# Kernel tuning notes

Measured on AMD Instinct MI355X. Metric: run time of the kernel, lower is better.

## Reference

```python
import jax, jax.numpy as jnp
import numpy as np
import math


def setup_inputs() -> dict:
    key = jax.random.key(0)
    ks = jax.random.split(key, 16)
    B, S, H, K, PREV = 32, 2048, 1024, 4, 2
    sc = 0.02
    return {
        "last_hidden": jax.random.normal(ks[0], (1, B, H), jnp.float32),
        "decoder_inputs": jax.random.normal(ks[1], (B, 1, H), jnp.float32),
        "encoder_outputs": jax.random.normal(ks[2], (B, S, H), jnp.float32),
        "attention_scores": jax.random.normal(ks[3], (PREV, B, 1, S), jnp.float32),
        "attention_mask": jnp.zeros((B, 1, S), jnp.float32),
        "evidence_scores": jax.random.uniform(ks[4], (B,), jnp.float32),
        "evidence_sentence_index": jax.random.randint(ks[5], (B, PREV), 0, S, dtype=jnp.int32),
        "W_ih": jax.random.normal(ks[6], (3 * H, H), jnp.float32) * sc,
        "W_hh": jax.random.normal(ks[7], (3 * H, H), jnp.float32) * sc,
        "b_ih": jax.random.normal(ks[8], (3 * H,), jnp.float32) * sc,
        "b_hh": jax.random.normal(ks[9], (3 * H,), jnp.float32) * sc,
        "Wk": jax.random.normal(ks[10], (H, H), jnp.float32) * sc,
        "bk": jnp.zeros((H,), jnp.float32),
        "Wv": jax.random.normal(ks[11], (H, H), jnp.float32) * sc,
        "bv": jnp.zeros((H,), jnp.float32),
        "topk": K,
    }


def _gru_step(x, h, W_ih, W_hh, b_ih, b_hh):
    # x, h: (B, H). PyTorch GRU cell math.
    gi = x @ W_ih.T + b_ih  # (B, 3H)
    gh = h @ W_hh.T + b_hh  # (B, 3H)
    i_r, i_z, i_n = jnp.split(gi, 3, axis=1)
    h_r, h_z, h_n = jnp.split(gh, 3, axis=1)
    r = jax.nn.sigmoid(i_r + h_r)
    z = jax.nn.sigmoid(i_z + h_z)
    n = jnp.tanh(i_n + r * h_n)
    return (1.0 - z) * n + z * h


def reference(last_hidden, decoder_inputs, encoder_outputs, attention_scores,
              attention_mask, evidence_scores, evidence_sentence_index,
              W_ih, W_hh, b_ih, b_hh, Wk, bk, Wv, bv, topk):
    B, S, H = encoder_outputs.shape
    K = topk
    R = B // K  # real batch (beam groups)

    key_eo = encoder_outputs @ Wk.T + bk    # (B, S, H)
    val_eo = encoder_outputs @ Wv.T + bv    # (B, S, H)

    h_new = _gru_step(decoder_inputs[:, 0], last_hidden[0], W_ih, W_hh, b_ih, b_hh)  # (B, H)
    output = h_new[:, None, :]              # (B, 1, H)

    attn_outputs = jnp.einsum('bih,bsh->bis', output, key_eo) / math.sqrt(H) + attention_mask  # (B,1,S)
    attn_alignment = jax.nn.softmax(attn_outputs, axis=-1)
    context = jnp.einsum('bis,bsh->bih', attn_alignment, val_eo)  # (B, 1, H)

    # top-k per beam, then joint rerank over topk*topk candidates per real example
    vals, idx = jax.lax.top_k(attn_alignment.reshape(R, K, S), K)  # (R, K, K), sorted desc
    scores = vals.reshape(B, K)
    sentences = idx.reshape(B, K)
    log_scores = -jnp.log(scores) + evidence_scores[:, None]       # (B, K)

    flat = log_scores.reshape(R, K * K)
    order = jnp.argsort(flat, axis=-1)[:, :K]                      # (R, K) ascending, stable
    new_evidence_scores = jnp.take_along_axis(flat, order, axis=1).reshape(B)
    s_flat = (order // K + jnp.arange(R)[:, None] * K).reshape(B)  # source beam in [0, B)
    r_flat = (order % K).reshape(B)

    sel_sent = sentences[s_flat, r_flat]                           # (B,)
    result = context[s_flat]                                       # (B, 1, H)
    hidden = h_new[s_flat][None]                                   # (1, B, H)
    new_evidence_sentence_index = jnp.concatenate(
        [evidence_sentence_index[s_flat], sel_sent[:, None].astype(evidence_sentence_index.dtype)], axis=1)
    new_attention_scores = jnp.concatenate(
        [attention_scores[:, s_flat], attn_outputs[s_flat][None]], axis=0)  # (prev+1, B, 1, S)
    new_attention_mask = attention_mask[s_flat]                    # (B, 1, S)

    return (result, hidden, new_evidence_sentence_index,
            new_attention_scores, new_attention_mask, new_evidence_scores)
```

## Files before the change

### kernel.cpp

```cpp
#include <hip/hip_runtime.h>
#include <hip/hip_bf16.h>
#include <cfloat>
#include <climits>
#include <cmath>

#define BB 32
#define SS 2048
#define HH 1024
#define KK 4
#define CH 32

__global__ __launch_bounds__(256) void gates_partial(
    const float* __restrict__ x, const float* __restrict__ h_old,
    const float* __restrict__ W_ih, const float* __restrict__ W_hh,
    float* __restrict__ part) {
  int t = threadIdx.x;
  int jb = blockIdx.x;
  int kc = blockIdx.y;
  int bq = blockIdx.z;
  int k0 = kc * 64;
  bool second = (jb >= 12);
  const float* A = (second ? h_old : x) + (size_t)(bq * 8) * HH;
  const float* W = second ? W_hh : W_ih;
  int j0 = jb * 256;
  int jr = j0 - (second ? 3072 : 0);
  const float* wp = W + (size_t)(jr + t) * HH + k0;
  float acc[8];
#pragma unroll
  for (int bi = 0; bi < 8; bi++) acc[bi] = 0.f;
#pragma unroll
  for (int kk = 0; kk < 64; kk += 4) {
    float4 wv = *(const float4*)(wp + kk);
#pragma unroll
    for (int bi = 0; bi < 8; bi++) {
      float4 a = *(const float4*)(A + (size_t)bi * HH + k0 + kk);
      acc[bi] += a.x * wv.x + a.y * wv.y + a.z * wv.z + a.w * wv.w;
    }
  }
  float* pb = part + ((size_t)kc * 32 + bq * 8) * 6144 + j0 + t;
#pragma unroll
  for (int bi = 0; bi < 8; bi++) pb[(size_t)bi * 6144] = acc[bi];
}

__global__ __launch_bounds__(256) void gru_pw(
    const float* __restrict__ part, const float* __restrict__ b_ih,
    const float* __restrict__ b_hh, const float* __restrict__ h_old,
    float* __restrict__ h_new) {
  int t = threadIdx.x;
  int b = blockIdx.x;
  int h = blockIdx.y * 256 + t;
  float s0 = 0.f, s1 = 0.f, s2 = 0.f, s3 = 0.f, s4 = 0.f, s5 = 0.f;
#pragma unroll
  for (int c = 0; c < 16; c++) {
    const float* p = part + ((size_t)c * 32 + b) * 6144;
    s0 += p[h];
    s1 += p[1024 + h];
    s2 += p[2048 + h];
    s3 += p[3072 + h];
    s4 += p[4096 + h];
    s5 += p[5120 + h];
  }
  float ir = s0 + b_ih[h], iz = s1 + b_ih[1024 + h], in_ = s2 + b_ih[2048 + h];
  float hr = s3 + b_hh[h], hz = s4 + b_hh[1024 + h], hn = s5 + b_hh[2048 + h];
  float r = 1.f / (1.f + expf(-(ir + hr)));
  float z = 1.f / (1.f + expf(-(iz + hz)));
  float n = tanhf(in_ + r * hn);
  h_new[b * HH + h] = (1.f - z) * n + z * h_old[b * HH + h];
}

__global__ __launch_bounds__(256) void q_partial(const float* __restrict__ hnew,
                                                 const float* __restrict__ Wk,
                                                 float* __restrict__ qpart) {
  int t = threadIdx.x;
  int n = blockIdx.x * 256 + t;
  int j0 = blockIdx.y * 32;
  int b0 = blockIdx.z * 8;
  float acc[8];
#pragma unroll
  for (int bi = 0; bi < 8; bi++) acc[bi] = 0.f;
#pragma unroll
  for (int j = 0; j < 32; j += 4) {
    float w0 = Wk[(size_t)(j0 + j + 0) * HH + n];
    float w1 = Wk[(size_t)(j0 + j + 1) * HH + n];
    float w2 = Wk[(size_t)(j0 + j + 2) * HH + n];
    float w3 = Wk[(size_t)(j0 + j + 3) * HH + n];
#pragma unroll
    for (int bi = 0; bi < 8; bi++) {
      float4 hv = *(const float4*)(hnew + (size_t)(b0 + bi) * HH + j0 + j);
      acc[bi] += hv.x * w0 + hv.y * w1 + hv.z * w2 + hv.w * w3;
    }
  }
  float* pb = qpart + ((size_t)blockIdx.y * 32 + b0) * 1024 + n;
#pragma unroll
  for (int bi = 0; bi < 8; bi++) pb[(size_t)bi * 1024] = acc[bi];
}

__global__ __launch_bounds__(256) void q_reduce(const float* __restrict__ qpart,
                                                float* __restrict__ q) {
  int t = threadIdx.x;
  int b = blockIdx.x >> 2;
  int n = (blockIdx.x & 3) * 256 + t;
  float s = 0.f;
#pragma unroll
  for (int jc = 0; jc < 32; jc++) s += qpart[((size_t)jc * 32 + b) * 1024 + n];
  q[b * HH + n] = s;
}

__global__ __launch_bounds__(256) void fused_attn(
    const float* __restrict__ eo, const float* __restrict__ q,
    const float* __restrict__ h_new, const float* __restrict__ bk,
    const float* __restrict__ mask, float* __restrict__ logits,
    float* __restrict__ c0part, float* __restrict__ msum_part) {
  __shared__ float q_lds[HH];
  __shared__ float wred[4];
  __shared__ float cacc[4][1024];
  __shared__ float cms[4][2];
  int b = blockIdx.y, sc = blockIdx.x, t = threadIdx.x;
  int w = t >> 6, lane = t & 63;
  {
    float4 qs = *(const float4*)(q + (size_t)b * HH + 4 * t);
    *(float4*)&q_lds[4 * t] = qs;
    float4 hv = *(const float4*)(h_new + (size_t)b * HH + 4 * t);
    float4 kv = *(const float4*)(bk + 4 * t);
    float p = hv.x * kv.x + hv.y * kv.y + hv.z * kv.z + hv.w * kv.w;
#pragma unroll
    for (int off = 32; off; off >>= 1) p += __shfl_xor(p, off);
    if (lane == 0) wred[w] = p;
  }
  __syncthreads();
  float hb = wred[0] + wred[1] + wred[2] + wred[3];
  float4 qv[4];
#pragma unroll
  for (int i = 0; i < 4; i++) qv[i] = *(const float4*)&q_lds[(i * 64 + lane) * 4];

  float m = -FLT_MAX, sum = 0.f;
  float4 acc[4];
#pragma unroll
  for (int i = 0; i < 4; i++) acc[i] = make_float4(0.f, 0.f, 0.f, 0.f);
  int rbase = sc * 64 + w * 16;
  for (int tile = 0; tile < 8; tile++) {
    int r0 = rbase + tile * 2;
    float4 rv[2][4];
#pragma unroll
    for (int rr = 0; rr < 2; rr++) {
      const float4* e4 = (const float4*)(eo + ((size_t)b * SS + r0 + rr) * HH);
#pragma unroll
      for (int i = 0; i < 4; i++) rv[rr][i] = e4[i * 64 + lane];
    }
    float p0 = 0.f, p1 = 0.f;
#pragma unroll
    for (int i = 0; i < 4; i++) {
      p0 += rv[0][i].x * qv[i].x + rv[0][i].y * qv[i].y +
            rv[0][i].z * qv[i].z + rv[0][i].w * qv[i].w;
      p1 += rv[1][i].x * qv[i].x + rv[1][i].y * qv[i].y +
            rv[1][i].z * qv[i].z + rv[1][i].w * qv[i].w;
    }
#pragma unroll
    for (int off = 32; off; off >>= 1) {
      p0 += __shfl_xor(p0, off);
      p1 += __shfl_xor(p1, off);
    }
    float lv0 = (p0 + hb) * 0.03125f + mask[(size_t)b * SS + r0];
    float lv1 = (p1 + hb) * 0.03125f + mask[(size_t)b * SS + r0 + 1];
    if (lane == 0) {
      logits[(size_t)b * SS + r0] = lv0;
      logits[(size_t)b * SS + r0 + 1] = lv1;
    }
    float m_new = fmaxf(m, fmaxf(lv0, lv1));
    float scale = expf(m - m_new);
    float w0 = expf(lv0 - m_new), w1 = expf(lv1 - m_new);
    sum = sum * scale + w0 + w1;
#pragma unroll
    for (int i = 0; i < 4; i++) {
      acc[i].x = acc[i].x * scale + w0 * rv[0][i].x + w1 * rv[1][i].x;
      acc[i].y = acc[i].y * scale + w0 * rv[0][i].y + w1 * rv[1][i].y;
      acc[i].z = acc[i].z * scale + w0 * rv[0][i].z + w1 * rv[1][i].z;
      acc[i].w = acc[i].w * scale + w0 * rv[0][i].w + w1 * rv[1][i].w;
    }
    m = m_new;
  }
#pragma unroll
  for (int i = 0; i < 4; i++) *(float4*)&cacc[w][i * 256 + lane * 4] = acc[i];
  if (lane == 0) { cms[w][0] = m; cms[w][1] = sum; }
  __syncthreads();
  float m0 = cms[0][0], m1 = cms[1][0], m2 = cms[2][0], m3 = cms[3][0];
  float mb = fmaxf(fmaxf(m0, m1), fmaxf(m2, m3));
  float wt0 = expf(m0 - mb), wt1 = expf(m1 - mb), wt2 = expf(m2 - mb),
        wt3 = expf(m3 - mb);
  float sb = cms[0][1] * wt0 + cms[1][1] * wt1 + cms[2][1] * wt2 + cms[3][1] * wt3;
  float4 a0 = *(float4*)&cacc[0][4 * t];
  float4 a1 = *(float4*)&cacc[1][4 * t];
  float4 a2 = *(float4*)&cacc[2][4 * t];
  float4 a3 = *(float4*)&cacc[3][4 * t];
  float4 r;
  r.x = wt0 * a0.x + wt1 * a1.x + wt2 * a2.x + wt3 * a3.x;
  r.y = wt0 * a0.y + wt1 * a1.y + wt2 * a2.y + wt3 * a3.y;
  r.z = wt0 * a0.z + wt1 * a1.z + wt2 * a2.z + wt3 * a3.z;
  r.w = wt0 * a0.w + wt1 * a1.w + wt2 * a2.w + wt3 * a3.w;
  *(float4*)(c0part + ((size_t)sc * 32 + b) * 1024 + 4 * t) = r;
  if (t == 0) {
    msum_part[((size_t)sc * 32 + b) * 2 + 0] = mb;
    msum_part[((size_t)sc * 32 + b) * 2 + 1] = sb;
  }
}

__device__ __forceinline__ bool vi_better(float av, int ai, float bv, int bi) {
  return av > bv || (av == bv && ai < bi);
}

__global__ __launch_bounds__(256) void attn_finish(
    const float* __restrict__ c0part, const float* __restrict__ msum_part,
    const float* __restrict__ logits, float* __restrict__ c0,
    float* __restrict__ scores, int* __restrict__ sent) {
  int bid = blockIdx.x, t = threadIdx.x;
  int b = (bid < 128) ? (bid >> 2) : (bid - 128);
  float m = -FLT_MAX;
  float ms[CH];
#pragma unroll
  for (int c = 0; c < CH; c++) {
    ms[c] = msum_part[((size_t)c * 32 + b) * 2 + 0];
    m = fmaxf(m, ms[c]);
  }
  float sum = 0.f;
  float wc[CH];
#pragma unroll
  for (int c = 0; c < CH; c++) {
    wc[c] = expf(ms[c] - m);
    sum += msum_part[((size_t)c * 32 + b) * 2 + 1] * wc[c];
  }
  float inv = 1.f / sum;

  if (bid < 128) {
    int h = (bid & 3) * 256 + t;
    float a = 0.f;
#pragma unroll
    for (int c = 0; c < CH; c++)
      a += wc[c] * c0part[((size_t)c * 32 + b) * 1024 + h];
    c0[(size_t)b * HH + h] = a * inv;
    return;
  }

  float tv0 = -FLT_MAX, tv1 = -FLT_MAX, tv2 = -FLT_MAX, tv3 = -FLT_MAX;
  int ti0 = INT_MAX, ti1 = INT_MAX, ti2 = INT_MAX, ti3 = INT_MAX;
#pragma unroll
  for (int it = 0; it < 8; it++) {
    int idx = it * 256 + t;
    float v = logits[(size_t)b * SS + idx];
    if (vi_better(v, idx, tv3, ti3)) {
      tv3 = v; ti3 = idx;
      if (vi_better(tv3, ti3, tv2, ti2)) { float fv = tv2; int fi = ti2; tv2 = tv3; ti2 = ti3; tv3 = fv; ti3 = fi; }
      if (vi_better(tv2, ti2, tv1, ti1)) { float fv = tv1; int fi = ti1; tv1 = tv2; ti1 = ti2; tv2 = fv; ti2 = fi; }
      if (vi_better(tv1, ti1, tv0, ti0)) { float fv = tv0; int fi = ti0; tv0 = tv1; ti0 = ti1; tv1 = fv; ti1 = fi; }
    }
  }
  __shared__ float sv[256][4];
  __shared__ int si[256][4];
  sv[t][0] = tv0; sv[t][1] = tv1; sv[t][2] = tv2; sv[t][3] = tv3;
  si[t][0] = ti0; si[t][1] = ti1; si[t][2] = ti2; si[t][3] = ti3;
  __syncthreads();
  for (int off = 128; off; off >>= 1) {
    if (t < off) {
      float bv0 = sv[t + off][0], bv1 = sv[t + off][1], bv2 = sv[t + off][2], bv3 = sv[t + off][3];
      int bi0 = si[t + off][0], bi1 = si[t + off][1], bi2 = si[t + off][2], bi3 = si[t + off][3];
      float mv0, mv1, mv2, mv3; int mi0, mi1, mi2, mi3;
      if (vi_better(tv0, ti0, bv3, bi3)) { mv0 = tv0; mi0 = ti0; } else { mv0 = bv3; mi0 = bi3; }
      if (vi_better(tv1, ti1, bv2, bi2)) { mv1 = tv1; mi1 = ti1; } else { mv1 = bv2; mi1 = bi2; }
      if (vi_better(tv2, ti2, bv1, bi1)) { mv2 = tv2; mi2 = ti2; } else { mv2 = bv1; mi2 = bi1; }
      if (vi_better(tv3, ti3, bv0, bi0)) { mv3 = tv3; mi3 = ti3; } else { mv3 = bv0; mi3 = bi0; }
      if (!vi_better(mv0, mi0, mv2, mi2)) { float fv = mv0; int fi = mi0; mv0 = mv2; mi0 = mi2; mv2 = fv; mi2 = fi; }
      if (!vi_better(mv1, mi1, mv3, mi3)) { float fv = mv1; int fi = mi1; mv1 = mv3; mi1 = mi3; mv3 = fv; mi3 = fi; }
      if (!vi_better(mv0, mi0, mv1, mi1)) { float fv = mv0; int fi = mi0; mv0 = mv1; mi0 = mi1; mv1 = fv; mi1 = fi; }
      if (!vi_better(mv2, mi2, mv3, mi3)) { float fv = mv2; int fi = mi2; mv2 = mv3; mi2 = mi3; mv3 = fv; mi3 = fi; }
      tv0 = mv0; tv1 = mv1; tv2 = mv2; tv3 = mv3;
      ti0 = mi0; ti1 = mi1; ti2 = mi2; ti3 = mi3;
      sv[t][0] = tv0; sv[t][1] = tv1; sv[t][2] = tv2; sv[t][3] = tv3;
      si[t][0] = ti0; si[t][1] = ti1; si[t][2] = ti2; si[t][3] = ti3;
    }
    __syncthreads();
  }
  if (t == 0) {
    scores[b * KK + 0] = expf(tv0 - m) * inv; sent[b * KK + 0] = ti0;
    scores[b * KK + 1] = expf(tv1 - m) * inv; sent[b * KK + 1] = ti1;
    scores[b * KK + 2] = expf(tv2 - m) * inv; sent[b * KK + 2] = ti2;
    scores[b * KK + 3] = expf(tv3 - m) * inv; sent[b * KK + 3] = ti3;
  }
}

__global__ __launch_bounds__(256) void ctx_sel_gather(
    const float* __restrict__ scores, const int* __restrict__ sent,
    const float* __restrict__ evidence, const int* __restrict__ esi,
    const float* __restrict__ Wv, const float* __restrict__ bvec,
    const float* __restrict__ c0, const float* __restrict__ hnew,
    const float* __restrict__ attn_in, const float* __restrict__ logits,
    const float* __restrict__ mask, float* __restrict__ out0,
    float* __restrict__ out1, float* __restrict__ out2,
    float* __restrict__ out3, float* __restrict__ out4,
    float* __restrict__ out5) {
  __shared__ int s_sh;
  __shared__ float cs[HH];
  int jq = blockIdx.x, b = blockIdx.y, t = threadIdx.x;
  if (t == 0) {
    int r = b >> 2, j = b & 3;
    float ls[16];
    bool used[16];
    for (int k1 = 0; k1 < 4; k1++)
      for (int k2 = 0; k2 < 4; k2++)
        ls[k1 * 4 + k2] = -logf(scores[(r * 4 + k1) * 4 + k2]) + evidence[r * 4 + k1];
    for (int i = 0; i < 16; i++) used[i] = false;
    int best = 0;
    float bvv = FLT_MAX;
    for (int jj = 0; jj <= j; jj++) {
      best = 0;
      bvv = FLT_MAX;
      for (int i = 0; i < 16; i++)
        if (!used[i] && ls[i] < bvv) { bvv = ls[i]; best = i; }
      used[best] = true;
    }
    int k1 = best >> 2, k2 = best & 3;
    int sSel = r * 4 + k1;
    s_sh = sSel;
    if (jq == 0) {
      out5[b] = bvv;
      out2[b * 3 + 0] = (float)esi[sSel * 2 + 0];
      out2[b * 3 + 1] = (float)esi[sSel * 2 + 1];
      out2[b * 3 + 2] = (float)sent[sSel * 4 + k2];
    }
  }
  __syncthreads();
  int s = s_sh;
  *(float4*)&cs[4 * t] = *(const float4*)(c0 + (size_t)s * HH + 4 * t);
  __syncthreads();
  {
    int j = jq * 256 + t;
    const float4* w4 = (const float4*)(Wv + (size_t)j * HH);
    float acc = bvec[j];
#pragma unroll 8
    for (int k4 = 0; k4 < 256; k4++) {
      float4 wv = w4[k4];
      float4 cc = *(const float4*)&cs[4 * k4];
      acc += wv.x * cc.x + wv.y * cc.y + wv.z * cc.z + wv.w * cc.w;
    }
    out0[(size_t)b * HH + j] = acc;
  }
  out1[(size_t)b * HH + jq * 256 + t] = hnew[(size_t)s * HH + jq * 256 + t];
#pragma unroll
  for (int p = 0; p < 2; p++) {
    *(float2*)(out3 + ((size_t)p * BB + b) * SS + jq * 512 + 2 * t) =
        *(const float2*)(attn_in + ((size_t)p * BB + s) * SS + jq * 512 + 2 * t);
  }
  *(float2*)(out3 + ((size_t)2 * BB + b) * SS + jq * 512 + 2 * t) =
      *(const float2*)(logits + (size_t)s * SS + jq * 512 + 2 * t);
  *(float2*)(out4 + (size_t)b * SS + jq * 512 + 2 * t) =
      *(const float2*)(mask + (size_t)s * SS + jq * 512 + 2 * t);
}

extern "C" void kernel_launch(void* const* d_in, const int* in_sizes, int n_in,
                              void* d_out, int out_size, void* d_ws, size_t ws_size,
                              hipStream_t stream) {
  const float* h_old = (const float*)d_in[0];
  const float* x     = (const float*)d_in[1];
  const float* eo    = (const float*)d_in[2];
  const float* attn_in = (const float*)d_in[3];
  const float* mask  = (const float*)d_in[4];
  const float* evidence = (const float*)d_in[5];
  const int*   esi   = (const int*)d_in[6];
  const float* W_ih  = (const float*)d_in[7];
  const float* W_hh  = (const float*)d_in[8];
  const float* b_ih  = (const float*)d_in[9];
  const float* b_hh  = (const float*)d_in[10];
  const float* Wk    = (const float*)d_in[11];
  const float* bk    = (const float*)d_in[12];
  const float* Wv    = (const float*)d_in[13];
  const float* bv    = (const float*)d_in[14];

  float* w = (float*)d_ws;
  float* h_new  = w + 0;
  float* q      = w + 32768;
  float* logits = w + 65536;
  float* scores = w + 131072;
  int*   sent   = (int*)(w + 131200);
  float* c0     = w + 131328;
  float* msum_part = w + 164096;
  float* c0part = w + 166144;
  float* gpart  = w + 1214720;
  float* qpart  = w + 4360448;

  float* out0 = (float*)d_out;
  float* out1 = out0 + 32768;
  float* out2 = out1 + 32768;
  float* out3 = out2 + 96;
  float* out4 = out3 + 196608;
  float* out5 = out4 + 65536;

  gates_partial<<<dim3(24, 16, 4), 256, 0, stream>>>(x, h_old, W_ih, W_hh, gpart);
  gru_pw<<<dim3(32, 4), 256, 0, stream>>>(gpart, b_ih, b_hh, h_old, h_new);
  q_partial<<<dim3(4, 32, 4), 256, 0, stream>>>(h_new, Wk, qpart);
  q_reduce<<<128, 256, 0, stream>>>(qpart, q);
  fused_attn<<<dim3(CH, BB), 256, 0, stream>>>(eo, q, h_new, bk, mask, logits,
                                               c0part, msum_part);
  attn_finish<<<160, 256, 0, stream>>>(c0part, msum_part, logits, c0, scores, sent);
  ctx_sel_gather<<<dim3(4, BB), 256, 0, stream>>>(
      scores, sent, evidence, esi, Wv, bv, c0, h_new, attn_in, logits, mask,
      out0, out1, out2, out3, out4, out5);
}
```

Before: 127.5 us.

## Fuse attention finish into selection/context kernel with wave-level top-k

```diff
diff --git a/kernel.cpp b/kernel.cpp
--- a/kernel.cpp
+++ b/kernel.cpp
@@ -208,44 +208,45 @@
   return av > bv || (av == bv && ai < bi);
 }
 
-__global__ __launch_bounds__(256) void attn_finish(
+__global__ __launch_bounds__(256) void tail_sel_ctx(
     const float* __restrict__ c0part, const float* __restrict__ msum_part,
-    const float* __restrict__ logits, float* __restrict__ c0,
-    float* __restrict__ scores, int* __restrict__ sent) {
-  int bid = blockIdx.x, t = threadIdx.x;
-  int b = (bid < 128) ? (bid >> 2) : (bid - 128);
+    const float* __restrict__ logits, const float* __restrict__ evidence,
+    const int* __restrict__ esi, const float* __restrict__ Wv,
+    const float* __restrict__ bvec, const float* __restrict__ hnew,
+    const float* __restrict__ attn_in, const float* __restrict__ mask,
+    float* __restrict__ out0, float* __restrict__ out1,
+    float* __restrict__ out2, float* __restrict__ out3,
+    float* __restrict__ out4, float* __restrict__ out5) {
+  __shared__ float tvs[4][4];
+  __shared__ int tis[4][4];
+  __shared__ float mrow[4], srow[4];
+  __shared__ int s_sh;
+  __shared__ float wc_lds[32];
+  __shared__ float cs[HH];
+  int jq = blockIdx.x, b = blockIdx.y, t = threadIdx.x;
+  int w = t >> 6, lane = t & 63;
+  int r = b >> 2;
+  int row = r * 4 + w;
+
   float m = -FLT_MAX;
-  float ms[CH];
+  float msv[CH];
 #pragma unroll
   for (int c = 0; c < CH; c++) {
-    ms[c] = msum_part[((size_t)c * 32 + b) * 2 + 0];
-    m = fmaxf(m, ms[c]);
+    msv[c] = msum_part[((size_t)c * 32 + row) * 2 + 0];
+    m = fmaxf(m, msv[c]);
   }
   float sum = 0.f;
-  float wc[CH];
-#pragma unroll
-  for (int c = 0; c < CH; c++) {
-    wc[c] = expf(ms[c] - m);
-    sum += msum_part[((size_t)c * 32 + b) * 2 + 1] * wc[c];
-  }
-  float inv = 1.f / sum;
-
-  if (bid < 128) {
-    int h = (bid & 3) * 256 + t;
-    float a = 0.f;
-#pragma unroll
-    for (int c = 0; c < CH; c++)
-      a += wc[c] * c0part[((size_t)c * 32 + b) * 1024 + h];
-    c0[(size_t)b * HH + h] = a * inv;
-    return;
-  }
-
+#pragma unroll
+  for (int c = 0; c < CH; c++)
+    sum += msum_part[((size_t)c * 32 + row) * 2 + 1] * expf(msv[c] - m);
+
+  const float* lrow = logits + (size_t)row * SS;
   float tv0 = -FLT_MAX, tv1 = -FLT_MAX, tv2 = -FLT_MAX, tv3 = -FLT_MAX;
   int ti0 = INT_MAX, ti1 = INT_MAX, ti2 = INT_MAX, ti3 = INT_MAX;
 #pragma unroll
-  for (int it = 0; it < 8; it++) {
-    int idx = it * 256 + t;
-    float v = logits[(size_t)b * SS + idx];
+  for (int it = 0; it < 32; it++) {
+    int idx = it * 64 + lane;
+    float v = lrow[idx];
     if (vi_better(v, idx, tv3, ti3)) {
       tv3 = v; ti3 = idx;
       if (vi_better(tv3, ti3, tv2, ti2)) { float fv = tv2; int fi = ti2; tv2 = tv3; ti2 = ti3; tv3 = fv; ti3 = fi; }
@@ -253,59 +254,42 @@
       if (vi_better(tv1, ti1, tv0, ti0)) { float fv = tv0; int fi = ti0; tv0 = tv1; ti0 = ti1; tv1 = fv; ti1 = fi; }
     }
   }
-  __shared__ float sv[256][4];
-  __shared__ int si[256][4];
-  sv[t][0] = tv0; sv[t][1] = tv1; sv[t][2] = tv2; sv[t][3] = tv3;
-  si[t][0] = ti0; si[t][1] = ti1; si[t][2] = ti2; si[t][3] = ti3;
-  __syncthreads();
-  for (int off = 128; off; off >>= 1) {
-    if (t < off) {
-      float bv0 = sv[t + off][0], bv1 = sv[t + off][1], bv2 = sv[t + off][2], bv3 = sv[t + off][3];
-      int bi0 = si[t + off][0], bi1 = si[t + off][1], bi2 = si[t + off][2], bi3 = si[t + off][3];
-      float mv0, mv1, mv2, mv3; int mi0, mi1, mi2, mi3;
-      if (vi_better(tv0, ti0, bv3, bi3)) { mv0 = tv0; mi0 = ti0; } else { mv0 = bv3; mi0 = bi3; }
-      if (vi_better(tv1, ti1, bv2, bi2)) { mv1 = tv1; mi1 = ti1; } else { mv1 = bv2; mi1 = bi2; }
-      if (vi_better(tv2, ti2, bv1, bi1)) { mv2 = tv2; mi2 = ti2; } else { mv2 = bv1; mi2 = bi1; }
-      if (vi_better(tv3, ti3, bv0, bi0)) { mv3 = tv3; mi3 = ti3; } else { mv3 = bv0; mi3 = bi0; }
-      if (!vi_better(mv0, mi0, mv2, mi2)) { float fv = mv0; int fi = mi0; mv0 = mv2; mi0 = mi2; mv2 = fv; mi2 = fi; }
-      if (!vi_better(mv1, mi1, mv3, mi3)) { float fv = mv1; int fi = mi1; mv1 = mv3; mi1 = mi3; mv3 = fv; mi3 = fi; }
-      if (!vi_better(mv0, mi0, mv1, mi1)) { float fv = mv0; int fi = mi0; mv0 = mv1; mi0 = mi1; mv1 = fv; mi1 = fi; }
-      if (!vi_better(mv2, mi2, mv3, mi3)) { float fv = mv2; int fi = mi2; mv2 = mv3; mi2 = mi3; mv3 = fv; mi3 = fi; }
-      tv0 = mv0; tv1 = mv1; tv2 = mv2; tv3 = mv3;
-      ti0 = mi0; ti1 = mi1; ti2 = mi2; ti3 = mi3;
-      sv[t][0] = tv0; sv[t][1] = tv1; sv[t][2] = tv2; sv[t][3] = tv3;
-      si[t][0] = ti0; si[t][1] = ti1; si[t][2] = ti2; si[t][3] = ti3;
-    }
-    __syncthreads();
-  }
+#pragma unroll
+  for (int off = 32; off; off >>= 1) {
+    float bv0 = __shfl_xor(tv0, off), bv1 = __shfl_xor(tv1, off),
+          bv2 = __shfl_xor(tv2, off), bv3 = __shfl_xor(tv3, off);
+    int bi0 = __shfl_xor(ti0, off), bi1 = __shfl_xor(ti1, off),
+        bi2 = __shfl_xor(ti2, off), bi3 = __shfl_xor(ti3, off);
+    float mv0, mv1, mv2, mv3; int mi0, mi1, mi2, mi3;
+    if (vi_better(tv0, ti0, bv3, bi3)) { mv0 = tv0; mi0 = ti0; } else { mv0 = bv3; mi0 = bi3; }
+    if (vi_better(tv1, ti1, bv2, bi2)) { mv1 = tv1; mi1 = ti1; } else { mv1 = bv2; mi1 = bi2; }
+    if (vi_better(tv2, ti2, bv1, bi1)) { mv2 = tv2; mi2 = ti2; } else { mv2 = bv1; mi2 = bi1; }
+    if (vi_better(tv3, ti3, bv0, bi0)) { mv3 = tv3; mi3 = ti3; } else { mv3 = bv0; mi3 = bi0; }
+    if (!vi_better(mv0, mi0, mv2, mi2)) { float fv = mv0; int fi = mi0; mv0 = mv2; mi0 = mi2; mv2 = fv; mi2 = fi; }
+    if (!vi_better(mv1, mi1, mv3, mi3)) { float fv = mv1; int fi = mi1; mv1 = mv3; mi1 = mi3; mv3 = fv; mi3 = fi; }
+    if (!vi_better(mv0, mi0, mv1, mi1)) { float fv = mv0; int fi = mi0; mv0 = mv1; mi0 = mi1; mv1 = fv; mi1 = fi; }
+    if (!vi_better(mv2, mi2, mv3, mi3)) { float fv = mv2; int fi = mi2; mv2 = mv3; mi2 = mi3; mv3 = fv; mi3 = fi; }
+    tv0 = mv0; tv1 = mv1; tv2 = mv2; tv3 = mv3;
+    ti0 = mi0; ti1 = mi1; ti2 = mi2; ti3 = mi3;
+  }
+  if (lane == 0) {
+    tvs[w][0] = tv0; tvs[w][1] = tv1; tvs[w][2] = tv2; tvs[w][3] = tv3;
+    tis[w][0] = ti0; tis[w][1] = ti1; tis[w][2] = ti2; tis[w][3] = ti3;
+    mrow[w] = m; srow[w] = sum;
+  }
+  __syncthreads();
+
   if (t == 0) {
-    scores[b * KK + 0] = expf(tv0 - m) * inv; sent[b * KK + 0] = ti0;
-    scores[b * KK + 1] = expf(tv1 - m) * inv; sent[b * KK + 1] = ti1;
-    scores[b * KK + 2] = expf(tv2 - m) * inv; sent[b * KK + 2] = ti2;
-    scores[b * KK + 3] = expf(tv3 - m) * inv; sent[b * KK + 3] = ti3;
-  }
-}
-
-__global__ __launch_bounds__(256) void ctx_sel_gather(
-    const float* __restrict__ scores, const int* __restrict__ sent,
-    const float* __restrict__ evidence, const int* __restrict__ esi,
-    const float* __restrict__ Wv, const float* __restrict__ bvec,
-    const float* __restrict__ c0, const float* __restrict__ hnew,
-    const float* __restrict__ attn_in, const float* __restrict__ logits,
-    const float* __restrict__ mask, float* __restrict__ out0,
-    float* __restrict__ out1, float* __restrict__ out2,
-    float* __restrict__ out3, float* __restrict__ out4,
-    float* __restrict__ out5) {
-  __shared__ int s_sh;
-  __shared__ float cs[HH];
-  int jq = blockIdx.x, b = blockIdx.y, t = threadIdx.x;
-  if (t == 0) {
-    int r = b >> 2, j = b & 3;
+    int j = b & 3;
     float ls[16];
     bool used[16];
-    for (int k1 = 0; k1 < 4; k1++)
-      for (int k2 = 0; k2 < 4; k2++)
-        ls[k1 * 4 + k2] = -logf(scores[(r * 4 + k1) * 4 + k2]) + evidence[r * 4 + k1];
+    for (int k1 = 0; k1 < 4; k1++) {
+      float inv1 = 1.f / srow[k1];
+      for (int k2 = 0; k2 < 4; k2++) {
+        float score = expf(tvs[k1][k2] - mrow[k1]) * inv1;
+        ls[k1 * 4 + k2] = -logf(score) + evidence[r * 4 + k1];
+      }
+    }
     for (int i = 0; i < 16; i++) used[i] = false;
     int best = 0;
     float bvv = FLT_MAX;
@@ -323,13 +307,29 @@
       out5[b] = bvv;
       out2[b * 3 + 0] = (float)esi[sSel * 2 + 0];
       out2[b * 3 + 1] = (float)esi[sSel * 2 + 1];
-      out2[b * 3 + 2] = (float)sent[sSel * 4 + k2];
+      out2[b * 3 + 2] = (float)tis[k1][k2];
     }
   }
   __syncthreads();
   int s = s_sh;
-  *(float4*)&cs[4 * t] = *(const float4*)(c0 + (size_t)s * HH + 4 * t);
-  __syncthreads();
+  float m_s = mrow[s & 3];
+  float inv_s = 1.f / srow[s & 3];
+  if (t < 32) wc_lds[t] = expf(msum_part[((size_t)t * 32 + s) * 2 + 0] - m_s);
+  __syncthreads();
+
+  {
+    float4 a = make_float4(0.f, 0.f, 0.f, 0.f);
+#pragma unroll
+    for (int c = 0; c < CH; c++) {
+      float4 v = *(const float4*)(c0part + ((size_t)c * 32 + s) * 1024 + 4 * t);
+      a.x += wc_lds[c] * v.x; a.y += wc_lds[c] * v.y;
+      a.z += wc_lds[c] * v.z; a.w += wc_lds[c] * v.w;
+    }
+    a.x *= inv_s; a.y *= inv_s; a.z *= inv_s; a.w *= inv_s;
+    *(float4*)&cs[4 * t] = a;
+  }
+  __syncthreads();
+
   {
     int j = jq * 256 + t;
     const float4* w4 = (const float4*)(Wv + (size_t)j * HH);
@@ -377,13 +377,10 @@
   float* h_new  = w + 0;
   float* q      = w + 32768;
   float* logits = w + 65536;
-  float* scores = w + 131072;
-  int*   sent   = (int*)(w + 131200);
-  float* c0     = w + 131328;
-  float* msum_part = w + 164096;
-  float* c0part = w + 166144;
-  float* gpart  = w + 1214720;
-  float* qpart  = w + 4360448;
+  float* msum_part = w + 131072;
+  float* c0part = w + 133120;
+  float* gpart  = w + 1181696;
+  float* qpart  = w + 4327424;
 
   float* out0 = (float*)d_out;
   float* out1 = out0 + 32768;
@@ -398,8 +395,7 @@
   q_reduce<<<128, 256, 0, stream>>>(qpart, q);
   fused_attn<<<dim3(CH, BB), 256, 0, stream>>>(eo, q, h_new, bk, mask, logits,
                                                c0part, msum_part);
-  attn_finish<<<160, 256, 0, stream>>>(c0part, msum_part, logits, c0, scores, sent);
-  ctx_sel_gather<<<dim3(4, BB), 256, 0, stream>>>(
-      scores, sent, evidence, esi, Wv, bv, c0, h_new, attn_in, logits, mask,
+  tail_sel_ctx<<<dim3(4, BB), 256, 0, stream>>>(
+      c0part, msum_part, logits, evidence, esi, Wv, bv, h_new, attn_in, mask,
       out0, out1, out2, out3, out4, out5);
 }
```

Result: slower. 136.2 us (+6.8%).
